# Kernel tuning notes

Measured on AMD Instinct MI355X. Metric: run time of the kernel, lower is better.

Reference implementation:

```python
import jax, jax.numpy as jnp
import numpy as np

B, W, F_IN = 128, 128, 64   # batch, window_size, num_features
N = 64                      # nodes per graph == num_features == tcn_out_channels
E = 4096                    # edges per graph
ED = 16                     # edge_feature_dim
H, C = 4, 32                # heads, gat_out_dim
FLAT = N * H * C            # 8192
HID = FLAT // 4             # 2048
LRELU_SLOPE = 0.01          # F.leaky_relu default
BN_EPS = 1e-5


def setup_inputs() -> dict:
    key = jax.random.key(0)
    ks = jax.random.split(key, 16)
    x = jax.random.normal(ks[0], (B, W, F_IN), jnp.float32)
    edge_index = jax.random.randint(ks[1], (2, E), 0, N)
    edge_attr = jax.random.normal(ks[2], (B, E, ED), jnp.float32)
    s = lambda k, shape, fan: jax.random.normal(k, shape, jnp.float32) / np.sqrt(fan)
    tcn_w = s(ks[3], (N, F_IN, 3), F_IN * 3)
    tcn_b = jnp.zeros((N,), jnp.float32)
    lin_l_w = s(ks[4], (H * C, W), W)
    lin_l_b = jnp.zeros((H * C,), jnp.float32)
    lin_e_w = s(ks[5], (H * C, ED), ED)
    lin_e_b = jnp.zeros((H * C,), jnp.float32)
    att = s(ks[6], (1, H, C), C)
    fc1_w = s(ks[7], (HID, FLAT), FLAT)
    fc1_b = jnp.zeros((HID,), jnp.float32)
    bn_g = jnp.ones((HID,), jnp.float32)
    bn_b = jnp.zeros((HID,), jnp.float32)
    fc2_w = s(ks[8], (2, HID), HID)
    fc2_b = jnp.zeros((2,), jnp.float32)
    return dict(x=x, edge_index=edge_index, edge_attr=edge_attr,
                tcn_w=tcn_w, tcn_b=tcn_b,
                lin_l_w=lin_l_w, lin_l_b=lin_l_b,
                lin_e_w=lin_e_w, lin_e_b=lin_e_b, att=att,
                fc1_w=fc1_w, fc1_b=fc1_b, bn_g=bn_g, bn_b=bn_b,
                fc2_w=fc2_w, fc2_b=fc2_b)


def reference(x, edge_index, edge_attr, tcn_w, tcn_b,
              lin_l_w, lin_l_b, lin_e_w, lin_e_b, att,
              fc1_w, fc1_b, bn_g, bn_b, fc2_w, fc2_b):
    # TCN: Conv1d(k=3, pad=1) over the window dim
    xt = jnp.transpose(x, (0, 2, 1))  # [B, F_IN, W]
    x_g = jax.lax.conv_general_dilated(
        xt, tcn_w, window_strides=(1,), padding=((1, 1),),
        dimension_numbers=('NCH', 'OIH', 'NCH')) + tcn_b[None, :, None]
    # x_g: [B, N, W] -> per-sample graph with N nodes, W-dim node features

    src, dst = edge_index[0], edge_index[1]

    def gat_one(xn, ea):
        # xn: [N, W], ea: [E, ED]
        h = (xn @ lin_l_w.T + lin_l_b).reshape(N, H, C)
        e = (ea @ lin_e_w.T + lin_e_b).reshape(E, H, C)
        xi = h[dst]               # [E, H, C] target node feats
        xj = h[src]               # [E, H, C] source node feats
        a = jax.nn.leaky_relu(xi + xj + e, LRELU_SLOPE)
        score = jnp.einsum('ehc,ohc->eh', a, att)  # [E, H]
        # segment softmax over edges grouped by destination node
        m = jax.ops.segment_max(score, dst, num_segments=N)
        m = jnp.where(jnp.isfinite(m), m, 0.0)
        ex = jnp.exp(score - m[dst])
        den = jax.ops.segment_sum(ex, dst, num_segments=N)
        alpha = ex / (den[dst] + 1e-16)            # [E, H]
        msg = xj * alpha[:, :, None]               # [E, H, C]
        out = jax.ops.segment_sum(msg, dst, num_segments=N)  # [N, H, C]
        return out.reshape(N, H * C)

    x_gat = jax.vmap(gat_one)(x_g, edge_attr)      # [B, N, H*C]
    x_gat = jax.nn.elu(x_gat)
    x_flat = x_gat.reshape(B, FLAT)

    h1 = x_flat @ fc1_w.T + fc1_b
    # BatchNorm1d in eval mode with fresh running stats (mean=0, var=1)
    h1 = h1 * (bn_g / jnp.sqrt(1.0 + BN_EPS)) + bn_b
    h1 = jax.nn.relu(h1)  # dropout is identity in eval
    logits = h1 @ fc2_w.T + fc2_b
    return logits
```

## Files before the change

kernel.cpp:

```cpp
#include <hip/hip_runtime.h>
#include <math.h>

#define BB   128
#define WW   128
#define FIN  64
#define NNODE 64
#define NE   4096
#define EDIM 16
#define NH   4
#define CDIM 32
#define HC   128
#define FLATD 8192
#define HIDD 2048

#define OFF_H    0u
#define OFF_P    1048576u
#define OFF_XGB  3211264u
#define OFF_BK   4259840u

typedef unsigned short u16;
typedef u16    u16x8  __attribute__((ext_vector_type(8)));
typedef u16    u16x4  __attribute__((ext_vector_type(4)));
typedef __bf16 bf16x8 __attribute__((ext_vector_type(8)));
typedef float  f32x4  __attribute__((ext_vector_type(4)));
typedef float  f32x16 __attribute__((ext_vector_type(16)));

__device__ __forceinline__ u16 f2bf(float f) {
    unsigned u = __float_as_uint(f);
    u += 0x7fffu + ((u >> 16) & 1u);
    return (u16)(u >> 16);
}
__device__ __forceinline__ void hilo(float v, u16* h, u16* l) {
    u16 hh = f2bf(v);
    float hf = __uint_as_float(((unsigned)hh) << 16);
    *h = hh;
    *l = f2bf(v - hf);
}

__global__ __launch_bounds__(256) void k0_bucket(
        const int* __restrict__ ei, int* __restrict__ bstart, int* __restrict__ blist)
{
    __shared__ int cnt[64];
    __shared__ int cur[65];
    const int t = threadIdx.x;
    if (t < 64) cnt[t] = 0;
    __syncthreads();
    for (int e = t; e < NE; e += 256) atomicAdd(&cnt[ei[NE + e]], 1);
    __syncthreads();
    if (t == 0) {
        int run = 0;
        for (int n = 0; n < 64; ++n) { cur[n] = run; run += cnt[n]; }
        cur[64] = run;
    }
    __syncthreads();
    if (t < 65) bstart[t] = cur[t];
    __syncthreads();
    for (int e = t; e < NE; e += 256) {
        int d = ei[NE + e], s = ei[e];
        int p = atomicAdd(&cur[d], 1);
        blist[p] = (e << 12) | (d << 6) | s;
    }
}

__global__ __launch_bounds__(256) void k1_tcn_linl(
        const float* __restrict__ x, const float* __restrict__ tcn_w,
        const float* __restrict__ tcn_b, const float* __restrict__ lin_l_w,
        const float* __restrict__ lin_l_b, float* __restrict__ h)
{
    __shared__ float xs[130*65];
    __shared__ float xg[32*132];
    const int b = blockIdx.x, half = blockIdx.y, t = threadIdx.x;
    const int n0 = half * 32;

    for (int idx = t; idx < 8192; idx += 256) {
        int w = idx >> 6, i = idx & 63;
        xs[(w+1)*65 + i] = x[b*8192 + idx];
    }
    if (t < 65) { xs[t] = 0.f; xs[129*65 + t] = 0.f; }
    __syncthreads();

    {
        const int nl = t >> 3;
        const int n  = n0 + nl;
        const int w0 = (t & 7) * 16;
        float acc[16];
        const float tb = tcn_b[n];
#pragma unroll
        for (int j = 0; j < 16; ++j) acc[j] = tb;
        for (int i = 0; i < 64; ++i) {
            const float t0 = tcn_w[n*192 + 3*i + 0];
            const float t1 = tcn_w[n*192 + 3*i + 1];
            const float t2 = tcn_w[n*192 + 3*i + 2];
            float a = xs[(w0+0)*65 + i];
            float c0 = xs[(w0+1)*65 + i];
#pragma unroll
            for (int dw = 0; dw < 16; ++dw) {
                float c = xs[(w0+dw+2)*65 + i];
                acc[dw] += a*t0 + c0*t1 + c*t2;
                a = c0; c0 = c;
            }
        }
#pragma unroll
        for (int dw = 0; dw < 16; ++dw) xg[nl*132 + w0 + dw] = acc[dw];
    }
    __syncthreads();

    {
        const int o2 = t & 63, ng = t >> 6;
        const int oA = o2, oB = o2 + 64;
        float accA[8], accB[8];
        const float lbA = lin_l_b[oA], lbB = lin_l_b[oB];
#pragma unroll
        for (int j = 0; j < 8; ++j) { accA[j] = lbA; accB[j] = lbB; }
        for (int c = 0; c < 32; ++c) {
            const float4 lwA = *(const float4*)&lin_l_w[oA*128 + c*4];
            const float4 lwB = *(const float4*)&lin_l_w[oB*128 + c*4];
#pragma unroll
            for (int nn = 0; nn < 8; ++nn) {
                const float4 xv = *(const float4*)&xg[(ng*8+nn)*132 + c*4];
                accA[nn] += xv.x*lwA.x + xv.y*lwA.y + xv.z*lwA.z + xv.w*lwA.w;
                accB[nn] += xv.x*lwB.x + xv.y*lwB.y + xv.z*lwB.z + xv.w*lwB.w;
            }
        }
#pragma unroll
        for (int nn = 0; nn < 8; ++nn) {
            const int n = n0 + ng*8 + nn;
            h[(b*64 + n)*128 + oA] = accA[nn];
            h[(b*64 + n)*128 + oB] = accB[nn];
        }
    }
}

#define CAPF 2560
__global__ __launch_bounds__(512, 1) void k2_fused(
        const float* __restrict__ hbase, const float* __restrict__ ea,
        const float* __restrict__ lin_e_w, const float* __restrict__ lin_e_b,
        const float* __restrict__ att, const int* __restrict__ bstart,
        const int* __restrict__ blist, u16* __restrict__ xgb)
{
    __shared__ float hbuf[64*132];
    __shared__ float scl[CAPF*4];
    __shared__ float Pm[4][32][68];
    __shared__ int   bst[33];
    const int b = blockIdx.x, half = blockIdx.y, t = threadIdx.x;
    const int lane = t & 63, wv = t >> 6, l32 = lane & 31, h5 = lane >> 5;

    for (int idx = t; idx < 8192; idx += 512) {
        const int o = idx & 127;
        hbuf[(idx>>7)*132 + o] = hbase[(size_t)b*8192 + idx] + 0.5f*lin_e_b[o];
    }
    for (int idx = t; idx < 4*32*68; idx += 512) ((float*)Pm)[idx] = 0.f;
    if (t < 33) bst[t] = bstart[half*32 + t];
    bf16x8 Ah[4], Al[4];
#pragma unroll
    for (int mt = 0; mt < 4; ++mt) {
        const float* wp = &lin_e_w[(mt*32 + l32)*16 + h5*8];
        const float4 w0 = *(const float4*)wp;
        const float4 w1 = *(const float4*)(wp + 4);
        u16 th[8], tl[8];
        hilo(w0.x,&th[0],&tl[0]); hilo(w0.y,&th[1],&tl[1]);
        hilo(w0.z,&th[2],&tl[2]); hilo(w0.w,&th[3],&tl[3]);
        hilo(w1.x,&th[4],&tl[4]); hilo(w1.y,&th[5],&tl[5]);
        hilo(w1.z,&th[6],&tl[6]); hilo(w1.w,&th[7],&tl[7]);
        u16x8 vh = { th[0],th[1],th[2],th[3],th[4],th[5],th[6],th[7] };
        u16x8 vl = { tl[0],tl[1],tl[2],tl[3],tl[4],tl[5],tl[6],tl[7] };
        Ah[mt] = *(bf16x8*)&vh;
        Al[mt] = *(bf16x8*)&vl;
    }
    float4 attv[4][4];
#pragma unroll
    for (int mt = 0; mt < 4; ++mt)
#pragma unroll
        for (int g = 0; g < 4; ++g)
            attv[mt][g] = *(const float4*)&att[mt*32 + g*8 + h5*4];
    __syncthreads();

    const int lo = bst[0], cnt = min(bst[32] - lo, CAPF);
    const int gcnt = (cnt + 31) >> 5;

    for (int g = wv; g < gcnt; g += 8) {
        const int idx = g*32 + l32;
        const bool valid = idx < cnt;
        const int pk = valid ? blist[lo + idx] : 0;
        const int sn = pk & 63, dd = (pk >> 6) & 63, e = pk >> 12;
        const float* eap = ea + ((size_t)b*NE + e)*16 + h5*8;
        const float4 v0 = *(const float4*)eap;
        const float4 v1 = *(const float4*)(eap + 4);
        u16 bh[8], bl[8];
        hilo(v0.x,&bh[0],&bl[0]); hilo(v0.y,&bh[1],&bl[1]);
        hilo(v0.z,&bh[2],&bl[2]); hilo(v0.w,&bh[3],&bl[3]);
        hilo(v1.x,&bh[4],&bl[4]); hilo(v1.y,&bh[5],&bl[5]);
        hilo(v1.z,&bh[6],&bl[6]); hilo(v1.w,&bh[7],&bl[7]);
        u16x8 vbh = { bh[0],bh[1],bh[2],bh[3],bh[4],bh[5],bh[6],bh[7] };
        u16x8 vbl = { bl[0],bl[1],bl[2],bl[3],bl[4],bl[5],bl[6],bl[7] };
        const bf16x8 Bh = *(bf16x8*)&vbh;
        const bf16x8 Bl = *(bf16x8*)&vbl;
        float hacc[4];
#pragma unroll
        for (int mt = 0; mt < 4; ++mt) {
            f32x16 D = {0.f,0.f,0.f,0.f,0.f,0.f,0.f,0.f,
                        0.f,0.f,0.f,0.f,0.f,0.f,0.f,0.f};
            D = __builtin_amdgcn_mfma_f32_32x32x16_bf16(Al[mt], Bh, D, 0, 0, 0);
            D = __builtin_amdgcn_mfma_f32_32x32x16_bf16(Ah[mt], Bl, D, 0, 0, 0);
            D = __builtin_amdgcn_mfma_f32_32x32x16_bf16(Ah[mt], Bh, D, 0, 0, 0);
            float s = 0.f;
#pragma unroll
            for (int g4 = 0; g4 < 4; ++g4) {
                const int ob = mt*32 + g4*8 + h5*4;
                const float4 hd = *(const float4*)&hbuf[dd*132 + ob];
                const float4 hs = *(const float4*)&hbuf[sn*132 + ob];
                float x0 = hd.x + hs.x + D[g4*4+0];
                float x1 = hd.y + hs.y + D[g4*4+1];
                float x2 = hd.z + hs.z + D[g4*4+2];
                float x3 = hd.w + hs.w + D[g4*4+3];
                x0 = fmaxf(x0, 0.01f*x0); x1 = fmaxf(x1, 0.01f*x1);
                x2 = fmaxf(x2, 0.01f*x2); x3 = fmaxf(x3, 0.01f*x3);
                const float4 a4 = attv[mt][g4];
                s += a4.x*x0 + a4.y*x1 + a4.z*x2 + a4.w*x3;
            }
            hacc[mt] = s;
        }
#pragma unroll
        for (int hh = 0; hh < 4; ++hh)
            hacc[hh] += __shfl_xor(hacc[hh], 32);
        if (h5 == 0 && valid)
            *(float4*)&scl[idx*4] = make_float4(hacc[0], hacc[1], hacc[2], hacc[3]);
    }
    __syncthreads();

    {
        const int pair = t >> 2, sub = t & 3;
        const int nl = pair >> 2, hh = pair & 3;
        const int s0 = bst[nl] - lo, s1 = bst[nl+1] - lo;
        float mx = -3.4e38f;
        for (int i = s0 + sub; i < s1; i += 4) mx = fmaxf(mx, scl[i*4 + hh]);
        mx = fmaxf(mx, __shfl_xor(mx, 1));
        mx = fmaxf(mx, __shfl_xor(mx, 2));
        float den = 0.f;
        for (int i = s0 + sub; i < s1; i += 4) {
            const float ex = __expf(scl[i*4 + hh] - mx);
            scl[i*4 + hh] = ex;
            den += ex;
        }
        den += __shfl_xor(den, 1);
        den += __shfl_xor(den, 2);
        const float rd = 1.0f / (den + 1e-16f);
        for (int i = s0 + sub; i < s1; i += 4) {
            const int src = blist[lo + i] & 63;
            atomicAdd(&Pm[hh][nl][src], scl[i*4 + hh] * rd);
        }
    }
    __syncthreads();

    if (wv < 4) {
        const int hh = wv;
        f32x16 D = {0.f,0.f,0.f,0.f,0.f,0.f,0.f,0.f,
                    0.f,0.f,0.f,0.f,0.f,0.f,0.f,0.f};
#pragma unroll
        for (int k0 = 0; k0 < 64; k0 += 16) {
            const float* pp = &Pm[hh][l32][k0 + h5*8];
            const float4 a0 = *(const float4*)pp;
            const float4 a1 = *(const float4*)(pp + 4);
            u16 ph[8], pl[8];
            hilo(a0.x,&ph[0],&pl[0]); hilo(a0.y,&ph[1],&pl[1]);
            hilo(a0.z,&ph[2],&pl[2]); hilo(a0.w,&ph[3],&pl[3]);
            hilo(a1.x,&ph[4],&pl[4]); hilo(a1.y,&ph[5],&pl[5]);
            hilo(a1.z,&ph[6],&pl[6]); hilo(a1.w,&ph[7],&pl[7]);
            u16x8 vph = { ph[0],ph[1],ph[2],ph[3],ph[4],ph[5],ph[6],ph[7] };
            u16x8 vpl = { pl[0],pl[1],pl[2],pl[3],pl[4],pl[5],pl[6],pl[7] };
            u16 hhv[8], hlv[8];
#pragma unroll
            for (int i = 0; i < 8; ++i) {
                const float v = hbuf[(k0 + h5*8 + i)*132 + hh*32 + l32];
                hilo(v, &hhv[i], &hlv[i]);
            }
            u16x8 vhh = { hhv[0],hhv[1],hhv[2],hhv[3],hhv[4],hhv[5],hhv[6],hhv[7] };
            u16x8 vhl = { hlv[0],hlv[1],hlv[2],hlv[3],hlv[4],hlv[5],hlv[6],hlv[7] };
            const bf16x8 Ph = *(bf16x8*)&vph, Pl = *(bf16x8*)&vpl;
            const bf16x8 Hh = *(bf16x8*)&vhh, Hl = *(bf16x8*)&vhl;
            D = __builtin_amdgcn_mfma_f32_32x32x16_bf16(Pl, Hh, D, 0, 0, 0);
            D = __builtin_amdgcn_mfma_f32_32x32x16_bf16(Ph, Hl, D, 0, 0, 0);
            D = __builtin_amdgcn_mfma_f32_32x32x16_bf16(Ph, Hh, D, 0, 0, 0);
        }
        const int c = l32, o = hh*32 + c;
        const float lb2 = 0.5f * lin_e_b[o];
#pragma unroll
        for (int r = 0; r < 16; ++r) {
            const int m = (r & 3) + 8*(r >> 2) + 4*h5;
            const float corr = (bst[m+1] > bst[m]) ? lb2 : 0.f;
            float v = D[r] - corr;
            v = v > 0.f ? v : expm1f(v);
            xgb[(size_t)b*8192 + (half*32 + m)*128 + o] = f2bf(v);
        }
    }
}

__global__ __launch_bounds__(256) void k3_fc1(
        const u16* __restrict__ xgb, const float* __restrict__ fc1_w,
        float* __restrict__ part)
{
    __shared__ u16 Ash[128*72];
    __shared__ u16 Bsh[32*72];
    const int jb = blockIdx.x, ks = blockIdx.y, t = threadIdx.x;
    const int j0 = jb*32, k0 = ks*1024;
    const int wave = t >> 6, lane = t & 63;
    const int quad = lane >> 4, l16 = lane & 15;
    const int wm = (wave & 1) * 64, wn = (wave >> 1) * 16;

    f32x4 acc[4];
#pragma unroll
    for (int i = 0; i < 4; ++i) acc[i] = (f32x4){0.f, 0.f, 0.f, 0.f};

    const int arow = t >> 1, acol = (t & 1) * 32;
    const int brow = t >> 3, bcol = (t & 7) * 8;

    for (int kc = 0; kc < 1024; kc += 64) {
        if (kc) __syncthreads();
        const u16* ap = xgb + (size_t)arow*FLATD + k0 + kc + acol;
#pragma unroll
        for (int qq = 0; qq < 4; ++qq)
            *(u16x8*)&Ash[arow*72 + acol + qq*8] = *(const u16x8*)(ap + qq*8);
        const float* bp = fc1_w + (size_t)(j0 + brow)*FLATD + k0 + kc + bcol;
        {
            float4 v0 = *(const float4*)(bp);
            float4 v1 = *(const float4*)(bp + 4);
            u16x8 u = { f2bf(v0.x), f2bf(v0.y), f2bf(v0.z), f2bf(v0.w),
                        f2bf(v1.x), f2bf(v1.y), f2bf(v1.z), f2bf(v1.w) };
            *(u16x8*)&Bsh[brow*72 + bcol] = u;
        }
        __syncthreads();
#pragma unroll
        for (int kk = 0; kk < 64; kk += 32) {
            bf16x8 af[4], bfr;
#pragma unroll
            for (int i = 0; i < 4; ++i)
                af[i] = *(const bf16x8*)&Ash[(wm + i*16 + l16)*72 + kk + quad*8];
            bfr = *(const bf16x8*)&Bsh[(wn + l16)*72 + kk + quad*8];
#pragma unroll
            for (int i = 0; i < 4; ++i)
                acc[i] = __builtin_amdgcn_mfma_f32_16x16x32_bf16(af[i], bfr, acc[i], 0, 0, 0);
        }
    }
#pragma unroll
    for (int i = 0; i < 4; ++i) {
        const int n = j0 + wn + l16;
#pragma unroll
        for (int r = 0; r < 4; ++r) {
            const int m = wm + i*16 + quad*4 + r;
            part[(size_t)ks*262144 + (size_t)m*HIDD + n] = acc[i][r];
        }
    }
}

__global__ __launch_bounds__(256) void k4_fc2(
        const float* __restrict__ part, const float* __restrict__ fc1_b,
        const float* __restrict__ bn_g, const float* __restrict__ bn_b,
        const float* __restrict__ fc2_w, const float* __restrict__ fc2_b,
        float* __restrict__ out)
{
    __shared__ float r0[256], r1[256];
    const int b = blockIdx.x, t = threadIdx.x;
    const float inv = 1.0f / sqrtf(1.0f + 1e-5f);
    float p0 = 0.f, p1 = 0.f;
    for (int j = t; j < 2048; j += 256) {
        float hv = 0.f;
#pragma unroll
        for (int s = 0; s < 8; ++s) hv += part[(size_t)s*262144 + (size_t)b*2048 + j];
        float v = (hv + fc1_b[j]) * (bn_g[j] * inv) + bn_b[j];
        v = fmaxf(v, 0.f);
        p0 += v * fc2_w[j];
        p1 += v * fc2_w[2048 + j];
    }
    r0[t] = p0; r1[t] = p1;
    __syncthreads();
    for (int s = 128; s > 0; s >>= 1) {
        if (t < s) { r0[t] += r0[t+s]; r1[t] += r1[t+s]; }
        __syncthreads();
    }
    if (t == 0) {
        out[b*2 + 0] = r0[0] + fc2_b[0];
        out[b*2 + 1] = r1[0] + fc2_b[1];
    }
}

extern "C" void kernel_launch(void* const* d_in, const int* in_sizes, int n_in,
                              void* d_out, int out_size, void* d_ws, size_t ws_size,
                              hipStream_t stream)
{
    const float* x       = (const float*)d_in[0];
    const int*   ei      = (const int*)  d_in[1];
    const float* ea      = (const float*)d_in[2];
    const float* tcn_w   = (const float*)d_in[3];
    const float* tcn_b   = (const float*)d_in[4];
    const float* lin_l_w = (const float*)d_in[5];
    const float* lin_l_b = (const float*)d_in[6];
    const float* lin_e_w = (const float*)d_in[7];
    const float* lin_e_b = (const float*)d_in[8];
    const float* att     = (const float*)d_in[9];
    const float* fc1_w   = (const float*)d_in[10];
    const float* fc1_b   = (const float*)d_in[11];
    const float* bn_g    = (const float*)d_in[12];
    const float* bn_b    = (const float*)d_in[13];
    const float* fc2_w   = (const float*)d_in[14];
    const float* fc2_b   = (const float*)d_in[15];

    float* ws     = (float*)d_ws;
    float* hbuf   = ws + OFF_H;
    float* part   = ws + OFF_P;
    u16*   xgb    = (u16*)(ws + OFF_XGB);
    int*   bstart = (int*)(ws + OFF_BK);
    int*   blist  = bstart + 80;
    float* out    = (float*)d_out;

    k0_bucket  <<<1, 256, 0, stream>>>(ei, bstart, blist);
    k1_tcn_linl<<<dim3(BB, 2), 256, 0, stream>>>(x, tcn_w, tcn_b, lin_l_w, lin_l_b, hbuf);
    k2_fused   <<<dim3(BB, 2), 512, 0, stream>>>(hbuf, ea, lin_e_w, lin_e_b, att,
                                                 bstart, blist, xgb);
    k3_fc1     <<<dim3(64, 8), 256, 0, stream>>>(xgb, fc1_w, part);
    k4_fc2     <<<BB, 256, 0, stream>>>(part, fc1_b, bn_g, bn_b, fc2_w, fc2_b, out);
}
```

Baseline: 247.2 us.

## Split GAT, fc1 and fc2 kernels into finer grids for more parallelism

The fused GAT kernel now splits each graph's destination nodes into four quarters instead of two. It uses 16x16 MFMA tiles spread over all eight waves and asks for two blocks per CU. The fc1 GEMM tiles shrink to 16 output columns, which doubles the block count, and the fc2 reduction is split four ways per sample and combined with atomics into an output zeroed by a memset. The goal is higher occupancy and more CU coverage on the MI355X. In exchange, each graph's h tile is loaded more often, the smaller tiles re-read fc1 inputs more, and there is an extra memset plus atomics.

```diff
diff --git a/kernel.cpp b/kernel.cpp
--- a/kernel.cpp
+++ b/kernel.cpp
@@ -131,26 +131,26 @@
     }
 }
 
-#define CAPF 2560
-__global__ __launch_bounds__(512, 1) void k2_fused(
+#define CAPQ 1280
+__global__ __launch_bounds__(512, 2) void k2_fused(
         const float* __restrict__ hbase, const float* __restrict__ ea,
         const float* __restrict__ lin_e_w, const float* __restrict__ lin_e_b,
         const float* __restrict__ att, const int* __restrict__ bstart,
         const int* __restrict__ blist, u16* __restrict__ xgb)
 {
     __shared__ float hbuf[64*132];
-    __shared__ float scl[CAPF*4];
-    __shared__ float Pm[4][32][68];
-    __shared__ int   bst[33];
-    const int b = blockIdx.x, half = blockIdx.y, t = threadIdx.x;
+    __shared__ float scl[CAPQ*4];
+    __shared__ float Pm[4][16][68];
+    __shared__ int   bst[17];
+    const int b = blockIdx.x, q = blockIdx.y, t = threadIdx.x;
     const int lane = t & 63, wv = t >> 6, l32 = lane & 31, h5 = lane >> 5;
 
     for (int idx = t; idx < 8192; idx += 512) {
         const int o = idx & 127;
         hbuf[(idx>>7)*132 + o] = hbase[(size_t)b*8192 + idx] + 0.5f*lin_e_b[o];
     }
-    for (int idx = t; idx < 4*32*68; idx += 512) ((float*)Pm)[idx] = 0.f;
-    if (t < 33) bst[t] = bstart[half*32 + t];
+    for (int idx = t; idx < 4*16*68; idx += 512) ((float*)Pm)[idx] = 0.f;
+    if (t < 17) bst[t] = bstart[q*16 + t];
     bf16x8 Ah[4], Al[4];
 #pragma unroll
     for (int mt = 0; mt < 4; ++mt) {
@@ -175,7 +175,7 @@
             attv[mt][g] = *(const float4*)&att[mt*32 + g*8 + h5*4];
     __syncthreads();
 
-    const int lo = bst[0], cnt = min(bst[32] - lo, CAPF);
+    const int lo = bst[0], cnt = min(bst[16] - lo, CAPQ);
     const int gcnt = (cnt + 31) >> 5;
 
     for (int g = wv; g < gcnt; g += 8) {
@@ -229,90 +229,86 @@
     __syncthreads();
 
     {
-        const int pair = t >> 2, sub = t & 3;
+        const int pair = t >> 3, sub = t & 7;
         const int nl = pair >> 2, hh = pair & 3;
         const int s0 = bst[nl] - lo, s1 = bst[nl+1] - lo;
         float mx = -3.4e38f;
-        for (int i = s0 + sub; i < s1; i += 4) mx = fmaxf(mx, scl[i*4 + hh]);
+        for (int i = s0 + sub; i < s1; i += 8) mx = fmaxf(mx, scl[i*4 + hh]);
         mx = fmaxf(mx, __shfl_xor(mx, 1));
         mx = fmaxf(mx, __shfl_xor(mx, 2));
+        mx = fmaxf(mx, __shfl_xor(mx, 4));
         float den = 0.f;
-        for (int i = s0 + sub; i < s1; i += 4) {
+        for (int i = s0 + sub; i < s1; i += 8) {
             const float ex = __expf(scl[i*4 + hh] - mx);
             scl[i*4 + hh] = ex;
             den += ex;
         }
         den += __shfl_xor(den, 1);
         den += __shfl_xor(den, 2);
+        den += __shfl_xor(den, 4);
         const float rd = 1.0f / (den + 1e-16f);
-        for (int i = s0 + sub; i < s1; i += 4) {
+        for (int i = s0 + sub; i < s1; i += 8) {
             const int src = blist[lo + i] & 63;
             atomicAdd(&Pm[hh][nl][src], scl[i*4 + hh] * rd);
         }
     }
     __syncthreads();
 
-    if (wv < 4) {
-        const int hh = wv;
-        f32x16 D = {0.f,0.f,0.f,0.f,0.f,0.f,0.f,0.f,
-                    0.f,0.f,0.f,0.f,0.f,0.f,0.f,0.f};
-#pragma unroll
-        for (int k0 = 0; k0 < 64; k0 += 16) {
-            const float* pp = &Pm[hh][l32][k0 + h5*8];
-            const float4 a0 = *(const float4*)pp;
-            const float4 a1 = *(const float4*)(pp + 4);
-            u16 ph[8], pl[8];
-            hilo(a0.x,&ph[0],&pl[0]); hilo(a0.y,&ph[1],&pl[1]);
-            hilo(a0.z,&ph[2],&pl[2]); hilo(a0.w,&ph[3],&pl[3]);
-            hilo(a1.x,&ph[4],&pl[4]); hilo(a1.y,&ph[5],&pl[5]);
-            hilo(a1.z,&ph[6],&pl[6]); hilo(a1.w,&ph[7],&pl[7]);
+    {
+        const int o0 = wv*16;
+        const int hh = wv >> 1;
+        const int quad = lane >> 4, l16 = lane & 15;
+        f32x4 D = (f32x4){0.f, 0.f, 0.f, 0.f};
+#pragma unroll
+        for (int k0 = 0; k0 < 64; k0 += 32) {
+            u16 ph[8], pl[8], bhv[8], blv[8];
+#pragma unroll
+            for (int j = 0; j < 8; ++j) {
+                const int k = k0 + quad*8 + j;
+                hilo(Pm[hh][l16][k], &ph[j], &pl[j]);
+                hilo(hbuf[k*132 + o0 + l16], &bhv[j], &blv[j]);
+            }
             u16x8 vph = { ph[0],ph[1],ph[2],ph[3],ph[4],ph[5],ph[6],ph[7] };
             u16x8 vpl = { pl[0],pl[1],pl[2],pl[3],pl[4],pl[5],pl[6],pl[7] };
-            u16 hhv[8], hlv[8];
-#pragma unroll
-            for (int i = 0; i < 8; ++i) {
-                const float v = hbuf[(k0 + h5*8 + i)*132 + hh*32 + l32];
-                hilo(v, &hhv[i], &hlv[i]);
-            }
-            u16x8 vhh = { hhv[0],hhv[1],hhv[2],hhv[3],hhv[4],hhv[5],hhv[6],hhv[7] };
-            u16x8 vhl = { hlv[0],hlv[1],hlv[2],hlv[3],hlv[4],hlv[5],hlv[6],hlv[7] };
+            u16x8 vbh = { bhv[0],bhv[1],bhv[2],bhv[3],bhv[4],bhv[5],bhv[6],bhv[7] };
+            u16x8 vbl = { blv[0],blv[1],blv[2],blv[3],blv[4],blv[5],blv[6],blv[7] };
             const bf16x8 Ph = *(bf16x8*)&vph, Pl = *(bf16x8*)&vpl;
-            const bf16x8 Hh = *(bf16x8*)&vhh, Hl = *(bf16x8*)&vhl;
-            D = __builtin_amdgcn_mfma_f32_32x32x16_bf16(Pl, Hh, D, 0, 0, 0);
-            D = __builtin_amdgcn_mfma_f32_32x32x16_bf16(Ph, Hl, D, 0, 0, 0);
-            D = __builtin_amdgcn_mfma_f32_32x32x16_bf16(Ph, Hh, D, 0, 0, 0);
-        }
-        const int c = l32, o = hh*32 + c;
+            const bf16x8 Hh = *(bf16x8*)&vbh, Hl = *(bf16x8*)&vbl;
+            D = __builtin_amdgcn_mfma_f32_16x16x32_bf16(Pl, Hh, D, 0, 0, 0);
+            D = __builtin_amdgcn_mfma_f32_16x16x32_bf16(Ph, Hl, D, 0, 0, 0);
+            D = __builtin_amdgcn_mfma_f32_16x16x32_bf16(Ph, Hh, D, 0, 0, 0);
+        }
+        const int o = o0 + l16;
         const float lb2 = 0.5f * lin_e_b[o];
 #pragma unroll
-        for (int r = 0; r < 16; ++r) {
-            const int m = (r & 3) + 8*(r >> 2) + 4*h5;
+        for (int r = 0; r < 4; ++r) {
+            const int m = quad*4 + r;
             const float corr = (bst[m+1] > bst[m]) ? lb2 : 0.f;
             float v = D[r] - corr;
             v = v > 0.f ? v : expm1f(v);
-            xgb[(size_t)b*8192 + (half*32 + m)*128 + o] = f2bf(v);
-        }
-    }
-}
-
-__global__ __launch_bounds__(256) void k3_fc1(
+            xgb[(size_t)b*8192 + (q*16 + m)*128 + o] = f2bf(v);
+        }
+    }
+}
+
+__global__ __launch_bounds__(256, 4) void k3_fc1(
         const u16* __restrict__ xgb, const float* __restrict__ fc1_w,
         float* __restrict__ part)
 {
     __shared__ u16 Ash[128*72];
-    __shared__ u16 Bsh[32*72];
+    __shared__ u16 Bsh[16*72];
     const int jb = blockIdx.x, ks = blockIdx.y, t = threadIdx.x;
-    const int j0 = jb*32, k0 = ks*1024;
+    const int j0 = jb*16, k0 = ks*1024;
     const int wave = t >> 6, lane = t & 63;
     const int quad = lane >> 4, l16 = lane & 15;
-    const int wm = (wave & 1) * 64, wn = (wave >> 1) * 16;
-
-    f32x4 acc[4];
-#pragma unroll
-    for (int i = 0; i < 4; ++i) acc[i] = (f32x4){0.f, 0.f, 0.f, 0.f};
+    const int wm = wave * 32;
+
+    f32x4 acc[2];
+#pragma unroll
+    for (int i = 0; i < 2; ++i) acc[i] = (f32x4){0.f, 0.f, 0.f, 0.f};
 
     const int arow = t >> 1, acol = (t & 1) * 32;
-    const int brow = t >> 3, bcol = (t & 7) * 8;
+    const int brow = t >> 4, bcol = (t & 15) * 4;
 
     for (int kc = 0; kc < 1024; kc += 64) {
         if (kc) __syncthreads();
@@ -322,28 +318,26 @@
             *(u16x8*)&Ash[arow*72 + acol + qq*8] = *(const u16x8*)(ap + qq*8);
         const float* bp = fc1_w + (size_t)(j0 + brow)*FLATD + k0 + kc + bcol;
         {
-            float4 v0 = *(const float4*)(bp);
-            float4 v1 = *(const float4*)(bp + 4);
-            u16x8 u = { f2bf(v0.x), f2bf(v0.y), f2bf(v0.z), f2bf(v0.w),
-                        f2bf(v1.x), f2bf(v1.y), f2bf(v1.z), f2bf(v1.w) };
-            *(u16x8*)&Bsh[brow*72 + bcol] = u;
+            float4 v = *(const float4*)bp;
+            u16x4 u = { f2bf(v.x), f2bf(v.y), f2bf(v.z), f2bf(v.w) };
+            *(u16x4*)&Bsh[brow*72 + bcol] = u;
         }
         __syncthreads();
 #pragma unroll
         for (int kk = 0; kk < 64; kk += 32) {
-            bf16x8 af[4], bfr;
-#pragma unroll
-            for (int i = 0; i < 4; ++i)
+            bf16x8 af[2], bfr;
+#pragma unroll
+            for (int i = 0; i < 2; ++i)
                 af[i] = *(const bf16x8*)&Ash[(wm + i*16 + l16)*72 + kk + quad*8];
-            bfr = *(const bf16x8*)&Bsh[(wn + l16)*72 + kk + quad*8];
-#pragma unroll
-            for (int i = 0; i < 4; ++i)
+            bfr = *(const bf16x8*)&Bsh[l16*72 + kk + quad*8];
+#pragma unroll
+            for (int i = 0; i < 2; ++i)
                 acc[i] = __builtin_amdgcn_mfma_f32_16x16x32_bf16(af[i], bfr, acc[i], 0, 0, 0);
         }
     }
 #pragma unroll
-    for (int i = 0; i < 4; ++i) {
-        const int n = j0 + wn + l16;
+    for (int i = 0; i < 2; ++i) {
+        const int n = j0 + l16;
 #pragma unroll
         for (int r = 0; r < 4; ++r) {
             const int m = wm + i*16 + quad*4 + r;
@@ -359,10 +353,12 @@
         float* __restrict__ out)
 {
     __shared__ float r0[256], r1[256];
-    const int b = blockIdx.x, t = threadIdx.x;
+    const int b = blockIdx.x, jq = blockIdx.y, t = threadIdx.x;
     const float inv = 1.0f / sqrtf(1.0f + 1e-5f);
     float p0 = 0.f, p1 = 0.f;
-    for (int j = t; j < 2048; j += 256) {
+#pragma unroll
+    for (int jj = 0; jj < 2; ++jj) {
+        const int j = jq*512 + jj*256 + t;
         float hv = 0.f;
 #pragma unroll
         for (int s = 0; s < 8; ++s) hv += part[(size_t)s*262144 + (size_t)b*2048 + j];
@@ -378,8 +374,10 @@
         __syncthreads();
     }
     if (t == 0) {
-        out[b*2 + 0] = r0[0] + fc2_b[0];
-        out[b*2 + 1] = r1[0] + fc2_b[1];
+        const float b0 = (jq == 0) ? fc2_b[0] : 0.f;
+        const float b1 = (jq == 0) ? fc2_b[1] : 0.f;
+        atomicAdd(&out[b*2 + 0], r0[0] + b0);
+        atomicAdd(&out[b*2 + 1], r1[0] + b1);
     }
 }
 
@@ -412,10 +410,12 @@
     int*   blist  = bstart + 80;
     float* out    = (float*)d_out;
 
+    hipMemsetAsync(out, 0, (size_t)out_size*sizeof(float), stream);
+
     k0_bucket  <<<1, 256, 0, stream>>>(ei, bstart, blist);
     k1_tcn_linl<<<dim3(BB, 2), 256, 0, stream>>>(x, tcn_w, tcn_b, lin_l_w, lin_l_b, hbuf);
-    k2_fused   <<<dim3(BB, 2), 512, 0, stream>>>(hbuf, ea, lin_e_w, lin_e_b, att,
+    k2_fused   <<<dim3(BB, 4), 512, 0, stream>>>(hbuf, ea, lin_e_w, lin_e_b, att,
                                                  bstart, blist, xgb);
-    k3_fc1     <<<dim3(64, 8), 256, 0, stream>>>(xgb, fc1_w, part);
-    k4_fc2     <<<BB, 256, 0, stream>>>(part, fc1_b, bn_g, bn_b, fc2_w, fc2_b, out);
-}
+    k3_fc1     <<<dim3(128, 8), 256, 0, stream>>>(xgb, fc1_w, part);
+    k4_fc2     <<<dim3(BB, 4), 256, 0, stream>>>(part, fc1_b, bn_g, bn_b, fc2_w, fc2_b, out);
+}
```

Result: slower. 270.1 us (+9.3%).
